# Kernel tuning notes

Measured on AMD Instinct MI355X. Metric: run time of the kernel, lower is better.

## Reference

```python
import jax, jax.numpy as jnp
import numpy as np

T, B, D, H = 512, 256, 256, 256


def setup_inputs() -> dict:
    key = jax.random.key(0)
    ks = jax.random.split(key, 10)
    # ragged lengths in [T//2, T], sorted descending as pack_padded_sequence requires
    lengths = np.sort(np.random.RandomState(0).randint(T // 2, T + 1, size=B))[::-1]
    # batch_sizes[t] = number of sequences still active at step t (non-increasing, >=1)
    batch_sizes = (lengths[None, :] > np.arange(T)[:, None]).sum(axis=1).astype(np.int32)
    batch_sizes = np.maximum(batch_sizes, 1)
    return {
        "input_x": jax.random.normal(ks[0], (T, B, D), jnp.float32),
        "h0": jax.random.normal(ks[1], (B, H), jnp.float32),
        "c0": jax.random.normal(ks[2], (B, H), jnp.float32),
        # variational dropout masks (precomputed, applied multiplicatively every step)
        "mask_x": (jax.random.uniform(ks[3], (B, D)) > 0.3).astype(jnp.float32) / 0.7,
        "mask_h": (jax.random.uniform(ks[4], (B, H)) > 0.3).astype(jnp.float32) / 0.7,
        "W_ih": jax.random.normal(ks[5], (4 * H, D), jnp.float32) * 0.05,
        "W_hh": jax.random.normal(ks[6], (4 * H, H), jnp.float32) * 0.05,
        "b_ih": jax.random.normal(ks[7], (4 * H,), jnp.float32) * 0.05,
        "b_hh": jax.random.normal(ks[8], (4 * H,), jnp.float32) * 0.05,
        "batch_sizes": jnp.asarray(batch_sizes),
    }


def reference(input_x, h0, c0, mask_x, mask_h, W_ih, W_hh, b_ih, b_hh, batch_sizes):
    # Forward (is_reversed=False) variational-dropout LSTM over a packed sequence.
    # Packed data is kept padded [T,B,*]; batch_sizes gives active rows per step.
    # Inactive rows keep their last-active hidden/cell state (== hn semantics).
    Bsz, Hid = h0.shape
    row = jnp.arange(Bsz)[:, None]

    def step(carry, inp):
        h, c = carry
        x_t, size = inp
        active = row < size  # [B,1]
        xi = x_t * mask_x            # input variational dropout
        hi = h * mask_h              # hidden variational dropout
        gates = xi @ W_ih.T + b_ih + hi @ W_hh.T + b_hh  # [B, 4H]
        i, f, g, o = jnp.split(gates, 4, axis=-1)
        c_new = jax.nn.sigmoid(f) * c + jax.nn.sigmoid(i) * jnp.tanh(g)
        h_new = jax.nn.sigmoid(o) * jnp.tanh(c_new)
        h = jnp.where(active, h_new, h)
        c = jnp.where(active, c_new, c)
        out = jnp.where(active, h_new, 0.0)  # padded positions zeroed (unused in pack)
        return (h, c), out

    (hn, cn), output = jax.lax.scan(step, (h0, c0), (input_x, batch_sizes))
    return output, hn, cn
```

## Files before the change

### kernel.cpp

```cpp
#include <hip/hip_runtime.h>
#include <hip/hip_bf16.h>

#define T_STEPS 512
#define BATCH   256
#define DIM     256
#define HID     256
#define DEPTH   4

using bf16x8  = __attribute__((ext_vector_type(8))) __bf16;
using floatx4 = __attribute__((ext_vector_type(4))) float;

__device__ __forceinline__ float sigf(float x)   { return 1.0f / (1.0f + __expf(-x)); }
__device__ __forceinline__ float tanh_f(float x) { return 1.0f - 2.0f / (1.0f + __expf(2.0f * x)); }

__device__ __forceinline__ bf16x8 cvt8(const float* p) {
  floatx4 a = *(const floatx4*)p;
  floatx4 b = *(const floatx4*)(p + 4);
  bf16x8 r;
  r[0]=(__bf16)a[0]; r[1]=(__bf16)a[1]; r[2]=(__bf16)a[2]; r[3]=(__bf16)a[3];
  r[4]=(__bf16)b[0]; r[5]=(__bf16)b[1]; r[6]=(__bf16)b[2]; r[7]=(__bf16)b[3];
  return r;
}

__global__ void init_ws(int* __restrict__ bar) { bar[blockIdx.x * 512 + threadIdx.x] = 0; }

__global__ __launch_bounds__(512, 2) void lstm_pc(
    const float* __restrict__ x, const float* __restrict__ h0,
    const float* __restrict__ c0,
    const float* __restrict__ mask_x, const float* __restrict__ mask_h,
    const float* __restrict__ W_ih, const float* __restrict__ W_hh,
    const float* __restrict__ b_ih, const float* __restrict__ b_hh,
    const int* __restrict__ bs_g,
    float* __restrict__ out, float* __restrict__ hn_out, float* __restrict__ cn_out,
    int* __restrict__ flg, float* __restrict__ ring,
    unsigned long long* __restrict__ inbox) {

  const int tid  = threadIdx.x;
  const int g    = blockIdx.x & 15;
  const int role = blockIdx.x >> 4;
  const int p    = role & 1;
  const int row_base = g * 16;
  const int lane = tid & 63;
  const int w    = tid >> 6;
  const int l15  = lane & 15;
  const int l4   = lane >> 4;

  __shared__ alignas(16) __bf16 s_ab[16 * 256];
  __shared__ int s_bs[T_STEPS];
  for (int i = tid; i < T_STEPS; i += 512) s_bs[i] = bs_g[i];
  __syncthreads();

  int* cons_flg_mine    = flg + (g * 2 + p) * 32;
  int* cons_flg_partner = flg + (g * 2 + (1 - p)) * 32;
  int* prod_flg_mine    = flg + 2048 + (g * 2 + p) * 32;
  float* ring_mine = ring + (size_t)(g * 2 + p) * (DEPTH * 8192);
  unsigned long long* inbox_mine    = inbox + (size_t)(g * 2 + p) * 1024;
  unsigned long long* inbox_partner = inbox + (size_t)(g * 2 + (1 - p)) * 1024;

  const int c_loc = w * 16 + l15;

  if (role >= 2) {
    bf16x8 wih_r[4][8];
    #pragma unroll
    for (int q = 0; q < 4; ++q) {
      const size_t wr = (size_t)(q * HID + p * 128 + c_loc) * DIM;
      #pragma unroll
      for (int m = 0; m < 8; ++m) wih_r[q][m] = cvt8(W_ih + wr + m * 32 + l4 * 8);
    }
    float bias[4];
    #pragma unroll
    for (int q = 0; q < 4; ++q) {
      const int bc = q * HID + p * 128 + c_loc;
      bias[q] = b_ih[bc] + b_hh[bc];
    }
    const int srow = tid & 15, scb = (tid >> 4) * 8;
    floatx4 mx0 = *(const floatx4*)(mask_x + (row_base + srow) * DIM + scb);
    floatx4 mx1 = *(const floatx4*)(mask_x + (row_base + srow) * DIM + scb + 4);
    const int soff = (srow * 512 + scb * 2) ^ ((srow & 7) << 4);

    for (int t = 0; t < T_STEPS; ++t) {
      if (s_bs[t] <= row_base) break;
      if (t >= DEPTH) {
        const int tgt = t - (DEPTH - 1);
        while (__hip_atomic_load(cons_flg_mine, __ATOMIC_RELAXED, __HIP_MEMORY_SCOPE_AGENT) < tgt) {}
      }
      const float* xp = x + ((size_t)t * BATCH + row_base + srow) * DIM + scb;
      floatx4 xa = *(const floatx4*)xp;
      floatx4 xb = *(const floatx4*)(xp + 4);
      bf16x8 xv;
      #pragma unroll
      for (int e = 0; e < 4; ++e) { xv[e] = (__bf16)(xa[e] * mx0[e]); xv[4 + e] = (__bf16)(xb[e] * mx1[e]); }
      *(bf16x8*)((char*)s_ab + soff) = xv;
      asm volatile("s_waitcnt lgkmcnt(0)" ::: "memory");
      __builtin_amdgcn_s_barrier();

      floatx4 a0, a1, a2, a3;
      a0 = a1 = a2 = a3 = (floatx4)(0.0f);
      #pragma unroll
      for (int m = 0; m < 8; ++m) {
        const int ab = (l15 * 512 + l4 * 16 + m * 64) ^ ((l15 & 7) << 4);
        bf16x8 ax = *(const bf16x8*)((const char*)s_ab + ab);
        a0 = __builtin_amdgcn_mfma_f32_16x16x32_bf16(ax, wih_r[0][m], a0, 0, 0, 0);
        a1 = __builtin_amdgcn_mfma_f32_16x16x32_bf16(ax, wih_r[1][m], a1, 0, 0, 0);
        a2 = __builtin_amdgcn_mfma_f32_16x16x32_bf16(ax, wih_r[2][m], a2, 0, 0, 0);
        a3 = __builtin_amdgcn_mfma_f32_16x16x32_bf16(ax, wih_r[3][m], a3, 0, 0, 0);
      }
      float* rs = ring_mine + (size_t)(t & (DEPTH - 1)) * 8192;
      #pragma unroll
      for (int e = 0; e < 4; ++e) {
        const int rb = (l4 * 4 + e) * 4;
        __hip_atomic_store(rs + (rb + 0) * 128 + c_loc, a0[e] + bias[0], __ATOMIC_RELAXED, __HIP_MEMORY_SCOPE_AGENT);
        __hip_atomic_store(rs + (rb + 1) * 128 + c_loc, a1[e] + bias[1], __ATOMIC_RELAXED, __HIP_MEMORY_SCOPE_AGENT);
        __hip_atomic_store(rs + (rb + 2) * 128 + c_loc, a2[e] + bias[2], __ATOMIC_RELAXED, __HIP_MEMORY_SCOPE_AGENT);
        __hip_atomic_store(rs + (rb + 3) * 128 + c_loc, a3[e] + bias[3], __ATOMIC_RELAXED, __HIP_MEMORY_SCOPE_AGENT);
      }
      asm volatile("s_waitcnt vmcnt(0)" ::: "memory");
      __builtin_amdgcn_s_barrier();
      if (tid == 0)
        __hip_atomic_store(prod_flg_mine, t + 1, __ATOMIC_RELAXED, __HIP_MEMORY_SCOPE_AGENT);
    }
    return;
  }

  const int c_own = p * 128 + c_loc;
  bf16x8 whh_r[4][8];
  #pragma unroll
  for (int q = 0; q < 4; ++q) {
    const size_t wr = (size_t)(q * HID + c_own) * HID;
    #pragma unroll
    for (int m = 0; m < 8; ++m) whh_r[q][m] = cvt8(W_hh + wr + m * 32 + l4 * 8);
  }
  float mh_c[4], h_[4], c_[4];
  #pragma unroll
  for (int e = 0; e < 4; ++e) {
    const int grow = row_base + l4 * 4 + e;
    mh_c[e] = mask_h[grow * HID + c_own];
    h_[e]   = h0[grow * HID + c_own];
    c_[e]   = c0[grow * HID + c_own];
  }
  const int sc_loc = tid >> 2;
  const int rq     = tid & 3;
  const int c_gs   = (1 - p) * 128 + sc_loc;
  float mh_s[4];
  #pragma unroll
  for (int e = 0; e < 4; ++e) mh_s[e] = mask_h[(row_base + rq * 4 + e) * HID + c_gs];

  while (__hip_atomic_load(prod_flg_mine, __ATOMIC_RELAXED, __HIP_MEMORY_SCOPE_AGENT) < 1) {}
  float xp_c[16];
  #pragma unroll
  for (int e = 0; e < 4; ++e)
    #pragma unroll
    for (int q = 0; q < 4; ++q)
      xp_c[e * 4 + q] = __hip_atomic_load(ring_mine + ((l4 * 4 + e) * 4 + q) * 128 + c_loc,
                                          __ATOMIC_RELAXED, __HIP_MEMORY_SCOPE_AGENT);

  for (int t = 0; t < T_STEPS; ++t) {
    const int bszt = s_bs[t];
    if (bszt <= row_base) {
      #pragma unroll
      for (int e = 0; e < 4; ++e)
        out[(size_t)t * (BATCH * HID) + (row_base + l4 * 4 + e) * HID + c_own] = 0.0f;
      continue;
    }
    const bool act_n = (t + 1 < T_STEPS) && (s_bs[t + 1] > row_base);

    #pragma unroll
    for (int e = 0; e < 4; ++e) {
      const int r = l4 * 4 + e;
      const int off = (r * 512 + c_own * 2) ^ ((r & 7) << 4);
      *(__bf16*)((char*)s_ab + off) = (__bf16)(h_[e] * mh_c[e]);
    }
    if (t == 0) {
      #pragma unroll
      for (int e = 0; e < 4; ++e) {
        const int r = rq * 4 + e;
        const float hv = h0[(row_base + r) * HID + c_gs] * mh_s[e];
        const int off = (r * 512 + c_gs * 2) ^ ((r & 7) << 4);
        *(__bf16*)((char*)s_ab + off) = (__bf16)hv;
      }
    } else {
      while (__hip_atomic_load(cons_flg_partner, __ATOMIC_RELAXED, __HIP_MEMORY_SCOPE_AGENT) < t) {}
      union { unsigned long long u; __bf16 b[4]; } pk;
      pk.u = __hip_atomic_load(inbox_mine + (size_t)(t & 1) * 512 + sc_loc * 4 + rq,
                               __ATOMIC_RELAXED, __HIP_MEMORY_SCOPE_AGENT);
      #pragma unroll
      for (int e = 0; e < 4; ++e) {
        const int r = rq * 4 + e;
        const float hv = (float)pk.b[e] * mh_s[e];
        const int off = (r * 512 + c_gs * 2) ^ ((r & 7) << 4);
        *(__bf16*)((char*)s_ab + off) = (__bf16)hv;
      }
    }
    float xp_n[16];
    if (act_n) {
      while (__hip_atomic_load(prod_flg_mine, __ATOMIC_RELAXED, __HIP_MEMORY_SCOPE_AGENT) < t + 2) {}
      const float* rs = ring_mine + (size_t)((t + 1) & (DEPTH - 1)) * 8192;
      #pragma unroll
      for (int e = 0; e < 4; ++e)
        #pragma unroll
        for (int q = 0; q < 4; ++q)
          xp_n[e * 4 + q] = __hip_atomic_load(rs + ((l4 * 4 + e) * 4 + q) * 128 + c_loc,
                                              __ATOMIC_RELAXED, __HIP_MEMORY_SCOPE_AGENT);
    }

    asm volatile("s_waitcnt lgkmcnt(0)" ::: "memory");
    __builtin_amdgcn_s_barrier();

    floatx4 a0, a1, a2, a3;
    a0 = a1 = a2 = a3 = (floatx4)(0.0f);
    #pragma unroll
    for (int m = 0; m < 8; ++m) {
      const int ab = (l15 * 512 + l4 * 16 + m * 64) ^ ((l15 & 7) << 4);
      bf16x8 ah = *(const bf16x8*)((const char*)s_ab + ab);
      a0 = __builtin_amdgcn_mfma_f32_16x16x32_bf16(ah, whh_r[0][m], a0, 0, 0, 0);
      a1 = __builtin_amdgcn_mfma_f32_16x16x32_bf16(ah, whh_r[1][m], a1, 0, 0, 0);
      a2 = __builtin_amdgcn_mfma_f32_16x16x32_bf16(ah, whh_r[2][m], a2, 0, 0, 0);
      a3 = __builtin_amdgcn_mfma_f32_16x16x32_bf16(ah, whh_r[3][m], a3, 0, 0, 0);
    }

    float o_[4];
    union { unsigned long long u; __bf16 b[4]; } hk;
    #pragma unroll
    for (int e = 0; e < 4; ++e) {
      const bool ract = (row_base + l4 * 4 + e) < bszt;
      const float iv = sigf(a0[e] + xp_c[e * 4 + 0]);
      const float fv = sigf(a1[e] + xp_c[e * 4 + 1]);
      const float gv = tanh_f(a2[e] + xp_c[e * 4 + 2]);
      const float ov = sigf(a3[e] + xp_c[e * 4 + 3]);
      const float cc = fv * c_[e] + iv * gv;
      const float hh = ov * tanh_f(cc);
      if (ract) { c_[e] = cc; h_[e] = hh; }
      o_[e] = ract ? hh : 0.0f;
      hk.b[e] = (__bf16)h_[e];
    }

    if (act_n) {
      __hip_atomic_store(inbox_partner + (size_t)((t + 1) & 1) * 512 + c_loc * 4 + l4, hk.u,
                         __ATOMIC_RELAXED, __HIP_MEMORY_SCOPE_AGENT);
      asm volatile("s_waitcnt vmcnt(0)" ::: "memory");
      __builtin_amdgcn_s_barrier();
      if (tid == 0)
        __hip_atomic_store(cons_flg_mine, t + 1, __ATOMIC_RELAXED, __HIP_MEMORY_SCOPE_AGENT);
    }

    #pragma unroll
    for (int e = 0; e < 4; ++e)
      out[(size_t)t * (BATCH * HID) + (row_base + l4 * 4 + e) * HID + c_own] = o_[e];

    if (act_n) {
      #pragma unroll
      for (int i = 0; i < 16; ++i) xp_c[i] = xp_n[i];
    }
  }

  #pragma unroll
  for (int e = 0; e < 4; ++e) {
    const int grow = row_base + l4 * 4 + e;
    hn_out[grow * HID + c_own] = h_[e];
    cn_out[grow * HID + c_own] = c_[e];
  }
}

extern "C" void kernel_launch(void* const* d_in, const int* in_sizes, int n_in,
                              void* d_out, int out_size, void* d_ws, size_t ws_size,
                              hipStream_t stream) {
  const float* x      = (const float*)d_in[0];
  const float* h0     = (const float*)d_in[1];
  const float* c0     = (const float*)d_in[2];
  const float* mask_x = (const float*)d_in[3];
  const float* mask_h = (const float*)d_in[4];
  const float* W_ih   = (const float*)d_in[5];
  const float* W_hh   = (const float*)d_in[6];
  const float* b_ih   = (const float*)d_in[7];
  const float* b_hh   = (const float*)d_in[8];
  const int*   bs     = (const int*)d_in[9];

  float* out = (float*)d_out;
  float* hn  = out + (size_t)T_STEPS * BATCH * HID;
  float* cn  = hn + (size_t)BATCH * HID;

  int*   flg  = (int*)d_ws;
  float* ring = (float*)((char*)d_ws + 16384);
  unsigned long long* inbox =
      (unsigned long long*)((char*)d_ws + 16384 + 4194304);

  init_ws<<<8, 512, 0, stream>>>(flg);
  lstm_pc<<<64, 512, 0, stream>>>(x, h0, c0, mask_x, mask_h, W_ih, W_hh,
                                  b_ih, b_hh, bs, out, hn, cn, flg, ring, inbox);
}
```

Before: 1.802 ms.

## Replace partner flag handshake with step-tagged inbox words and reorder ring prefetch

Each hidden-state exchange word now carries the step number in its low 32 bits next to two bf16 values, so the consumer polls the data itself and skips the separate partner flag. This removes a serial flag round trip and the vmcnt wait plus barrier before publishing. The next-step input prefetch moves ahead of the exchange wait so it can overlap it, and a single barrier at the end of each step replaces the old one. The cost is doubling the inbox payload width, software bf16 packing, and a wider init kernel that also zeroes the inbox. Launch bounds change to one block per CU.

```diff
diff --git a/kernel.cpp b/kernel.cpp
--- a/kernel.cpp
+++ b/kernel.cpp
@@ -9,6 +9,8 @@
 
 using bf16x8  = __attribute__((ext_vector_type(8))) __bf16;
 using floatx4 = __attribute__((ext_vector_type(4))) float;
+typedef unsigned long long u64;
+typedef unsigned int u32;
 
 __device__ __forceinline__ float sigf(float x)   { return 1.0f / (1.0f + __expf(-x)); }
 __device__ __forceinline__ float tanh_f(float x) { return 1.0f - 2.0f / (1.0f + __expf(2.0f * x)); }
@@ -21,10 +23,22 @@
   r[4]=(__bf16)b[0]; r[5]=(__bf16)b[1]; r[6]=(__bf16)b[2]; r[7]=(__bf16)b[3];
   return r;
 }
-
-__global__ void init_ws(int* __restrict__ bar) { bar[blockIdx.x * 512 + threadIdx.x] = 0; }
-
-__global__ __launch_bounds__(512, 2) void lstm_pc(
+__device__ __forceinline__ u32 f2bf(float f) {
+  union { float f; u32 u; } v; v.f = f;
+  u32 lsb = (v.u >> 16) & 1;
+  return (v.u + 0x7fff + lsb) >> 16;
+}
+__device__ __forceinline__ float bf2f(u32 u) {
+  union { u32 u; float f; } v; v.u = u << 16; return v.f;
+}
+
+__global__ void init_ws(int* __restrict__ flg, u64* __restrict__ inbox) {
+  const int idx = blockIdx.x * 256 + threadIdx.x;
+  if (idx < 4096) flg[idx] = 0;
+  if (idx < 65536) inbox[idx] = 0ull;
+}
+
+__global__ __launch_bounds__(512, 1) void lstm_pk(
     const float* __restrict__ x, const float* __restrict__ h0,
     const float* __restrict__ c0,
     const float* __restrict__ mask_x, const float* __restrict__ mask_h,
@@ -32,8 +46,7 @@
     const float* __restrict__ b_ih, const float* __restrict__ b_hh,
     const int* __restrict__ bs_g,
     float* __restrict__ out, float* __restrict__ hn_out, float* __restrict__ cn_out,
-    int* __restrict__ flg, float* __restrict__ ring,
-    unsigned long long* __restrict__ inbox) {
+    int* __restrict__ flg, float* __restrict__ ring, u64* __restrict__ inbox) {
 
   const int tid  = threadIdx.x;
   const int g    = blockIdx.x & 15;
@@ -50,12 +63,11 @@
   for (int i = tid; i < T_STEPS; i += 512) s_bs[i] = bs_g[i];
   __syncthreads();
 
-  int* cons_flg_mine    = flg + (g * 2 + p) * 32;
-  int* cons_flg_partner = flg + (g * 2 + (1 - p)) * 32;
-  int* prod_flg_mine    = flg + 2048 + (g * 2 + p) * 32;
+  int* cons_flg_mine = flg + (g * 2 + p) * 32;
+  int* prod_flg_mine = flg + 2048 + (g * 2 + p) * 32;
   float* ring_mine = ring + (size_t)(g * 2 + p) * (DEPTH * 8192);
-  unsigned long long* inbox_mine    = inbox + (size_t)(g * 2 + p) * 1024;
-  unsigned long long* inbox_partner = inbox + (size_t)(g * 2 + (1 - p)) * 1024;
+  u64* inbox_mine    = inbox + (size_t)(g * 2 + p) * 2048;
+  u64* inbox_partner = inbox + (size_t)(g * 2 + (1 - p)) * 2048;
 
   const int c_loc = w * 16 + l15;
 
@@ -146,6 +158,7 @@
   for (int e = 0; e < 4; ++e) mh_s[e] = mask_h[(row_base + rq * 4 + e) * HID + c_gs];
 
   while (__hip_atomic_load(prod_flg_mine, __ATOMIC_RELAXED, __HIP_MEMORY_SCOPE_AGENT) < 1) {}
+  asm volatile("" ::: "memory");
   float xp_c[16];
   #pragma unroll
   for (int e = 0; e < 4; ++e)
@@ -170,6 +183,20 @@
       const int off = (r * 512 + c_own * 2) ^ ((r & 7) << 4);
       *(__bf16*)((char*)s_ab + off) = (__bf16)(h_[e] * mh_c[e]);
     }
+
+    float xp_n[16];
+    if (act_n) {
+      while (__hip_atomic_load(prod_flg_mine, __ATOMIC_RELAXED, __HIP_MEMORY_SCOPE_AGENT) < t + 2) {}
+      asm volatile("" ::: "memory");
+      const float* rs = ring_mine + (size_t)((t + 1) & (DEPTH - 1)) * 8192;
+      #pragma unroll
+      for (int e = 0; e < 4; ++e)
+        #pragma unroll
+        for (int q = 0; q < 4; ++q)
+          xp_n[e * 4 + q] = __hip_atomic_load(rs + ((l4 * 4 + e) * 4 + q) * 128 + c_loc,
+                                              __ATOMIC_RELAXED, __HIP_MEMORY_SCOPE_AGENT);
+    }
+
     if (t == 0) {
       #pragma unroll
       for (int e = 0; e < 4; ++e) {
@@ -179,28 +206,23 @@
         *(__bf16*)((char*)s_ab + off) = (__bf16)hv;
       }
     } else {
-      while (__hip_atomic_load(cons_flg_partner, __ATOMIC_RELAXED, __HIP_MEMORY_SCOPE_AGENT) < t) {}
-      union { unsigned long long u; __bf16 b[4]; } pk;
-      pk.u = __hip_atomic_load(inbox_mine + (size_t)(t & 1) * 512 + sc_loc * 4 + rq,
-                               __ATOMIC_RELAXED, __HIP_MEMORY_SCOPE_AGENT);
+      const u64* ib = inbox_mine + (size_t)(t & 1) * 1024 + sc_loc * 8 + rq * 2;
+      u64 pk0, pk1;
+      do {
+        pk0 = __hip_atomic_load(ib,     __ATOMIC_RELAXED, __HIP_MEMORY_SCOPE_AGENT);
+        pk1 = __hip_atomic_load(ib + 1, __ATOMIC_RELAXED, __HIP_MEMORY_SCOPE_AGENT);
+      } while (!__all(((u32)pk0 == (u32)t) && ((u32)pk1 == (u32)t)));
+      float hv[4];
+      hv[0] = bf2f((u32)(pk0 >> 32) & 0xffffu) * mh_s[0];
+      hv[1] = bf2f((u32)(pk0 >> 48))           * mh_s[1];
+      hv[2] = bf2f((u32)(pk1 >> 32) & 0xffffu) * mh_s[2];
+      hv[3] = bf2f((u32)(pk1 >> 48))           * mh_s[3];
       #pragma unroll
       for (int e = 0; e < 4; ++e) {
         const int r = rq * 4 + e;
-        const float hv = (float)pk.b[e] * mh_s[e];
         const int off = (r * 512 + c_gs * 2) ^ ((r & 7) << 4);
-        *(__bf16*)((char*)s_ab + off) = (__bf16)hv;
-      }
-    }
-    float xp_n[16];
-    if (act_n) {
-      while (__hip_atomic_load(prod_flg_mine, __ATOMIC_RELAXED, __HIP_MEMORY_SCOPE_AGENT) < t + 2) {}
-      const float* rs = ring_mine + (size_t)((t + 1) & (DEPTH - 1)) * 8192;
-      #pragma unroll
-      for (int e = 0; e < 4; ++e)
-        #pragma unroll
-        for (int q = 0; q < 4; ++q)
-          xp_n[e * 4 + q] = __hip_atomic_load(rs + ((l4 * 4 + e) * 4 + q) * 128 + c_loc,
-                                              __ATOMIC_RELAXED, __HIP_MEMORY_SCOPE_AGENT);
+        *(__bf16*)((char*)s_ab + off) = (__bf16)hv[e];
+      }
     }
 
     asm volatile("s_waitcnt lgkmcnt(0)" ::: "memory");
@@ -219,7 +241,6 @@
     }
 
     float o_[4];
-    union { unsigned long long u; __bf16 b[4]; } hk;
     #pragma unroll
     for (int e = 0; e < 4; ++e) {
       const bool ract = (row_base + l4 * 4 + e) < bszt;
@@ -231,14 +252,15 @@
       const float hh = ov * tanh_f(cc);
       if (ract) { c_[e] = cc; h_[e] = hh; }
       o_[e] = ract ? hh : 0.0f;
-      hk.b[e] = (__bf16)h_[e];
     }
 
     if (act_n) {
-      __hip_atomic_store(inbox_partner + (size_t)((t + 1) & 1) * 512 + c_loc * 4 + l4, hk.u,
-                         __ATOMIC_RELAXED, __HIP_MEMORY_SCOPE_AGENT);
-      asm volatile("s_waitcnt vmcnt(0)" ::: "memory");
-      __builtin_amdgcn_s_barrier();
+      u64* ob = inbox_partner + (size_t)((t + 1) & 1) * 1024 + c_loc * 8 + l4 * 2;
+      const u64 tag = (u32)(t + 1);
+      u64 w0 = tag | ((u64)f2bf(h_[0]) << 32) | ((u64)f2bf(h_[1]) << 48);
+      u64 w1 = tag | ((u64)f2bf(h_[2]) << 32) | ((u64)f2bf(h_[3]) << 48);
+      __hip_atomic_store(ob,     w0, __ATOMIC_RELAXED, __HIP_MEMORY_SCOPE_AGENT);
+      __hip_atomic_store(ob + 1, w1, __ATOMIC_RELAXED, __HIP_MEMORY_SCOPE_AGENT);
       if (tid == 0)
         __hip_atomic_store(cons_flg_mine, t + 1, __ATOMIC_RELAXED, __HIP_MEMORY_SCOPE_AGENT);
     }
@@ -246,6 +268,8 @@
     #pragma unroll
     for (int e = 0; e < 4; ++e)
       out[(size_t)t * (BATCH * HID) + (row_base + l4 * 4 + e) * HID + c_own] = o_[e];
+
+    __builtin_amdgcn_s_barrier();
 
     if (act_n) {
       #pragma unroll
@@ -279,12 +303,11 @@
   float* hn  = out + (size_t)T_STEPS * BATCH * HID;
   float* cn  = hn + (size_t)BATCH * HID;
 
-  int*   flg  = (int*)d_ws;
+  int* flg  = (int*)d_ws;
   float* ring = (float*)((char*)d_ws + 16384);
-  unsigned long long* inbox =
-      (unsigned long long*)((char*)d_ws + 16384 + 4194304);
-
-  init_ws<<<8, 512, 0, stream>>>(flg);
-  lstm_pc<<<64, 512, 0, stream>>>(x, h0, c0, mask_x, mask_h, W_ih, W_hh,
+  u64* inbox = (u64*)((char*)d_ws + 16384 + 4194304);
+
+  init_ws<<<256, 256, 0, stream>>>(flg, inbox);
+  lstm_pk<<<64, 512, 0, stream>>>(x, h0, c0, mask_x, mask_h, W_ih, W_hh,
                                   b_ih, b_hh, bs, out, hn, cn, flg, ring, inbox);
 }
```

Result: slower. 1.935 ms (+7.4%).
